# Performance work log

Measured on AMD Instinct MI355X. Metric: run time of the kernel, lower is better.

The kernel has to match this reference:

```python
import jax, jax.numpy as jnp
import numpy as np

B, Q, K, C, H = 4, 1024, 1024, 1024, 16
L = C            # latent_dim (== in_dim per module construction)
CH = L // H      # head_dim = 64


def _ln(x, w, b):
    m = jnp.mean(x, -1, keepdims=True)
    v = jnp.mean((x - m) ** 2, -1, keepdims=True)
    return (x - m) * jax.lax.rsqrt(v + 1e-5) * w + b


def setup_inputs() -> dict:
    key = jax.random.key(0)
    ks = jax.random.split(key, 16)
    s = 0.02
    return {
        "queries": jax.random.normal(ks[0], (B, Q, C), jnp.float32),
        "contexts": jax.random.normal(ks[1], (B, K, C), jnp.float32),
        "queries_hidden": jax.random.normal(ks[2], (B, Q, L), jnp.float32),
        "sa_norm_w": jnp.ones((C,), jnp.float32),
        "sa_norm_b": jnp.zeros((C,), jnp.float32),
        "sa_qkv_w": jax.random.normal(ks[3], (C, 2 * L + C), jnp.float32) * s,
        "sa_out_w": jax.random.normal(ks[4], (C, C), jnp.float32) * s,
        "sa_out_b": jnp.zeros((C,), jnp.float32),
        "ca_norm_w": jnp.ones((C,), jnp.float32),
        "ca_norm_b": jnp.zeros((C,), jnp.float32),
        "gru_w_ih": jax.random.normal(ks[5], (3 * L, C), jnp.float32) * s,
        "gru_w_hh": jax.random.normal(ks[6], (3 * L, L), jnp.float32) * s,
        "gru_b_ih": jnp.zeros((3 * L,), jnp.float32),
        "gru_b_hh": jnp.zeros((3 * L,), jnp.float32),
        "ca_k_w": jax.random.normal(ks[7], (C, L), jnp.float32) * s,
        "ca_v_w": jax.random.normal(ks[8], (C, C), jnp.float32) * s,
        "ca_out_w": jax.random.normal(ks[9], (C, C), jnp.float32) * s,
        "ca_out_b": jnp.zeros((C,), jnp.float32),
        "ln1_w": jnp.ones((C,), jnp.float32),
        "ln1_b": jnp.zeros((C,), jnp.float32),
        "lin1_w": jax.random.normal(ks[10], (C, 2 * C), jnp.float32) * s,
        "ln2_w": jnp.ones((2 * C,), jnp.float32),
        "ln2_b": jnp.zeros((2 * C,), jnp.float32),
        "lin2_w": jax.random.normal(ks[11], (2 * C, C), jnp.float32) * s,
    }


def reference(queries, contexts, queries_hidden,
              sa_norm_w, sa_norm_b, sa_qkv_w, sa_out_w, sa_out_b,
              ca_norm_w, ca_norm_b, gru_w_ih, gru_w_hh, gru_b_ih, gru_b_hh,
              ca_k_w, ca_v_w, ca_out_w, ca_out_b,
              ln1_w, ln1_b, lin1_w, ln2_w, ln2_b, lin2_w):
    scale = 1.0 / jnp.sqrt(jnp.asarray(C, queries.dtype))

    # ---- SelfAttention (pre-norm, residual) ----
    xn = _ln(queries, sa_norm_w, sa_norm_b)
    qkv = (xn @ sa_qkv_w).reshape(B, Q, H, -1)          # [B,Q,H, 2*CH + C/H]
    q, k, v = jnp.split(qkv, [CH, 2 * CH], axis=-1)
    e = jnp.einsum('nqhc,nkhc->nhqk', q, k) * scale
    a = jax.nn.softmax(e, axis=-1)
    o = jnp.einsum('nhqk,nkhc->nqhc', a, v).reshape(B, Q, C)
    x = o @ sa_out_w + sa_out_b + queries

    # ---- AttentionDynamicQuery (GRU-updated queries, cross-attn) ----
    x_pre = x
    xn = _ln(x, ca_norm_w, ca_norm_b)
    xf = xn.reshape(B * Q, C)
    hf = queries_hidden.reshape(B * Q, L)
    gi = xf @ gru_w_ih.T + gru_b_ih                     # [BQ, 3L]
    gh = hf @ gru_w_hh.T + gru_b_hh
    gir, giz, gin = jnp.split(gi, 3, axis=-1)
    ghr, ghz, ghn = jnp.split(gh, 3, axis=-1)
    r = jax.nn.sigmoid(gir + ghr)
    z = jax.nn.sigmoid(giz + ghz)
    n = jnp.tanh(gin + r * ghn)
    h = (1.0 - z) * n + z * hf                          # PyTorch GRUCell update
    qh = h.reshape(B, Q, H, CH)                         # new queries_hidden

    kk = (contexts @ ca_k_w).reshape(B, K, H, CH)
    vv = (contexts @ ca_v_w).reshape(B, K, H, C // H)
    energy = jnp.einsum('nqhc,nkhc->nhqk', qh, kk)      # returned UNscaled
    att = jax.nn.softmax(energy * scale, axis=-1)
    o = jnp.einsum('nhqk,nkhc->nqhc', att, vv).reshape(B, Q, C)
    x = o @ ca_out_w + ca_out_b + x_pre

    # ---- MLP: LN -> SiLU -> Linear -> LN -> SiLU -> Linear, residual ----
    m = jax.nn.silu(_ln(x, ln1_w, ln1_b)) @ lin1_w
    m = jax.nn.silu(_ln(m, ln2_w, ln2_b)) @ lin2_w
    out = x + m                                         # dropout(p=0) = identity
    return (out, energy, qh)
```

## Files before the change

kernel.cpp:

```cpp
#include <hip/hip_runtime.h>
#include <hip/hip_bf16.h>
#include <math.h>

static constexpr float SCALE = 0.03125f;

typedef __attribute__((ext_vector_type(4))) float f32x4;
typedef __attribute__((ext_vector_type(8))) __bf16 bf16x8;
typedef __attribute__((ext_vector_type(4))) __bf16 bf16x4;

__device__ __forceinline__ void g2l16(const void* g, void* l) {
  __builtin_amdgcn_global_load_lds(
      (const __attribute__((address_space(1))) unsigned int*)g,
      (__attribute__((address_space(3))) unsigned int*)l,
      16, 0, 0);
}

__device__ __forceinline__ void wtrans_tile(
    const float* __restrict__ src, __bf16* __restrict__ dst,
    int Kd, int N, int tid, float (*tile)[65]) {
  int t = threadIdx.x;
  int ntx = N >> 6;
  int n0 = (tid % ntx) * 64, k0 = (tid / ntx) * 64;
  #pragma unroll
  for (int i = 0; i < 16; ++i) {
    int idx = i * 256 + t; int r = idx >> 6, c = idx & 63;
    tile[r][c] = src[(size_t)(k0 + r) * N + n0 + c];
  }
  __syncthreads();
  #pragma unroll
  for (int i = 0; i < 16; ++i) {
    int idx = i * 256 + t; int r = idx >> 6, c = idx & 63;
    dst[(size_t)(n0 + r) * Kd + k0 + c] = (__bf16)tile[c][r];
  }
}

__global__ __launch_bounds__(256) void prep_crit(
    const float* __restrict__ sa_qkv_w,
    const float* __restrict__ queries, const float* __restrict__ sa_norm_w,
    const float* __restrict__ sa_norm_b,
    __bf16* __restrict__ qkvT, __bf16* __restrict__ xnB) {
  int bid = blockIdx.x;
  int t = threadIdx.x;
  if (bid < 768) {
    __shared__ float tile[64][65];
    wtrans_tile(sa_qkv_w, qkvT, 1024, 3072, bid, tile);
    return;
  }
  int row = bid - 768;
  int c = t * 4;
  float4 v = *(const float4*)(queries + (size_t)row * 1024 + c);
  float s = v.x + v.y + v.z + v.w;
  float s2 = v.x*v.x + v.y*v.y + v.z*v.z + v.w*v.w;
  #pragma unroll
  for (int off = 32; off > 0; off >>= 1) {
    s += __shfl_xor(s, off);
    s2 += __shfl_xor(s2, off);
  }
  __shared__ float red[4], red2[4];
  int wv = t >> 6;
  if ((t & 63) == 0) { red[wv] = s; red2[wv] = s2; }
  __syncthreads();
  float S  = red[0] + red[1] + red[2] + red[3];
  float S2 = red2[0] + red2[1] + red2[2] + red2[3];
  float mean = S / 1024.f;
  float var = S2 / 1024.f - mean * mean;
  float rs = rsqrtf(var + 1e-5f);
  float vv[4] = {v.x, v.y, v.z, v.w};
  bf16x4 o;
  #pragma unroll
  for (int j = 0; j < 4; ++j)
    o[j] = (__bf16)((vv[j] - mean) * rs * sa_norm_w[c+j] + sa_norm_b[c+j]);
  *(bf16x4*)(xnB + (size_t)row * 1024 + c) = o;
}

template <int NV>
__global__ __launch_bounds__(256) void ln_bf16(
    const float* __restrict__ xf, const __bf16* __restrict__ xb,
    const float* __restrict__ w, const float* __restrict__ b,
    __bf16* __restrict__ out, int silu) {
  const int D = NV * 1024;
  int row = blockIdx.x, t = threadIdx.x;
  float vals[NV * 4];
  float s = 0.f, s2 = 0.f;
  #pragma unroll
  for (int i = 0; i < NV; ++i) {
    int c = (i * 256 + t) * 4;
    float4 v;
    if (xf) {
      v = *(const float4*)(xf + (size_t)row * D + c);
    } else {
      bf16x4 vb = *(const bf16x4*)(xb + (size_t)row * D + c);
      v = make_float4((float)vb[0], (float)vb[1], (float)vb[2], (float)vb[3]);
    }
    vals[i*4+0] = v.x; vals[i*4+1] = v.y; vals[i*4+2] = v.z; vals[i*4+3] = v.w;
    s += v.x + v.y + v.z + v.w;
    s2 += v.x*v.x + v.y*v.y + v.z*v.z + v.w*v.w;
  }
  #pragma unroll
  for (int off = 32; off > 0; off >>= 1) {
    s += __shfl_xor(s, off);
    s2 += __shfl_xor(s2, off);
  }
  __shared__ float red[4], red2[4];
  int wv = t >> 6;
  if ((t & 63) == 0) { red[wv] = s; red2[wv] = s2; }
  __syncthreads();
  float S  = red[0] + red[1] + red[2] + red[3];
  float S2 = red2[0] + red2[1] + red2[2] + red2[3];
  float mean = S / D;
  float var = S2 / D - mean * mean;
  float rs = rsqrtf(var + 1e-5f);
  #pragma unroll
  for (int i = 0; i < NV; ++i) {
    int c = (i * 256 + t) * 4;
    bf16x4 o;
    #pragma unroll
    for (int j = 0; j < 4; ++j) {
      float v = (vals[i*4+j] - mean) * rs * w[c+j] + b[c+j];
      if (silu) v = v / (1.f + __expf(-v));
      o[j] = (__bf16)v;
    }
    *(bf16x4*)(out + (size_t)row * D + c) = o;
  }
}

__device__ __forceinline__ void gemm_body(
    __bf16* __restrict__ sm,
    const __bf16* __restrict__ A, long long lda,
    const __bf16* __restrict__ B, long long ldb,
    float* __restrict__ outF, __bf16* __restrict__ outB, long long ldc,
    const float* __restrict__ bias, const float* __restrict__ res,
    int K, int bm, int bn, __bf16* __restrict__ VTout, int vmode) {
  __bf16* Asm0 = sm;
  __bf16* Bsm0 = sm + 8192;
  __bf16* Asm1 = sm + 16384;
  __bf16* Bsm1 = sm + 24576;
  int t = threadIdx.x;
  int lane = t & 63, w = t >> 6;
  int l15 = lane & 15, kg = lane >> 4;
  int wm = (w >> 1) * 64, wn = (w & 1) * 64;

  f32x4 acc[4][4];
  #pragma unroll
  for (int i = 0; i < 4; ++i)
    #pragma unroll
    for (int j = 0; j < 4; ++j) acc[i][j] = (f32x4)(0.0f);

  const __bf16* ga[4]; const __bf16* gb[4];
  int lo[4];
  #pragma unroll
  for (int i = 0; i < 4; ++i) {
    int slot = i * 256 + t;
    int row = slot >> 3, s = slot & 7;
    int sx = s ^ (row & 7);
    ga[i] = A + (size_t)(bm + row) * lda + (sx << 3);
    gb[i] = B + (size_t)(bn + row) * ldb + (sx << 3);
    lo[i] = (i * 256 + w * 64) << 3;
  }

  auto STAGE = [&](__bf16* As, __bf16* Bs, int k0) {
    #pragma unroll
    for (int i = 0; i < 4; ++i) g2l16(ga[i] + k0, As + lo[i]);
    #pragma unroll
    for (int i = 0; i < 4; ++i) g2l16(gb[i] + k0, Bs + lo[i]);
  };
  auto COMPUTE = [&](const __bf16* As, const __bf16* Bs) {
    #pragma unroll
    for (int kk = 0; kk < 2; ++kk) {
      bf16x8 af[4], bfr[4];
      #pragma unroll
      for (int mi = 0; mi < 4; ++mi) {
        int row = wm + mi * 16 + l15;
        int ks = kk * 4 + kg;
        af[mi] = *(const bf16x8*)(As + row * 64 + ((ks ^ (row & 7)) << 3));
      }
      #pragma unroll
      for (int ni = 0; ni < 4; ++ni) {
        int row = wn + ni * 16 + l15;
        int ks = kk * 4 + kg;
        bfr[ni] = *(const bf16x8*)(Bs + row * 64 + ((ks ^ (row & 7)) << 3));
      }
      #pragma unroll
      for (int mi = 0; mi < 4; ++mi)
        #pragma unroll
        for (int ni = 0; ni < 4; ++ni)
          acc[mi][ni] = __builtin_amdgcn_mfma_f32_16x16x32_bf16(
              af[mi], bfr[ni], acc[mi][ni], 0, 0, 0);
    }
  };
  #define GEMM_SYNC() do { \
    asm volatile("s_waitcnt vmcnt(0)" ::: "memory"); \
    __builtin_amdgcn_s_barrier(); \
    __builtin_amdgcn_sched_barrier(0); \
  } while (0)

  STAGE(Asm0, Bsm0, 0);
  GEMM_SYNC();
  int nk = K >> 6;
  for (int kt = 0; kt + 2 < nk; kt += 2) {
    STAGE(Asm1, Bsm1, (kt + 1) << 6);
    COMPUTE(Asm0, Bsm0);
    GEMM_SYNC();
    STAGE(Asm0, Bsm0, (kt + 2) << 6);
    COMPUTE(Asm1, Bsm1);
    GEMM_SYNC();
  }
  STAGE(Asm1, Bsm1, (nk - 1) << 6);
  COMPUTE(Asm0, Bsm0);
  GEMM_SYNC();
  COMPUTE(Asm1, Bsm1);
  #undef GEMM_SYNC

  int cw = bn + wn;
  int isV = 0;
  if (vmode == 1)      isV = (cw % 192) == 128;
  else if (vmode == 2) isV = cw >= 1024;

  if (isV) {
    int h = (vmode == 1) ? (cw / 192) : ((cw - 1024) >> 6);
    int rowb = bm + wm;
    int b = rowb >> 10, k0 = rowb & 1023;
    __bf16* scr = (w < 2 ? Asm0 : Bsm0) + (w & 1) * 4096;
    #pragma unroll
    for (int mi = 0; mi < 4; ++mi) {
      #pragma unroll
      for (int ni = 0; ni < 4; ++ni) {
        int d = ni * 16 + l15;
        int sw = (d & 7) << 3;
        #pragma unroll
        for (int r = 0; r < 4; ++r) {
          int kl = mi * 16 + kg * 4 + r;
          scr[d * 64 + (kl ^ sw)] = (__bf16)acc[mi][ni][r];
        }
      }
    }
    #pragma unroll
    for (int i = 0; i < 8; ++i) {
      int idx = i * 64 + lane;
      int d = idx >> 3, kc = (idx & 7) * 8;
      bf16x8 v = *(const bf16x8*)&scr[d * 64 + (kc ^ ((d & 7) << 3))];
      *(bf16x8*)(VTout + ((size_t)((b * 16 + h) * 64 + d) << 10) + k0 + kc) = v;
    }
    return;
  }

  #pragma unroll
  for (int mi = 0; mi < 4; ++mi) {
    #pragma unroll
    for (int ni = 0; ni < 4; ++ni) {
      int rbase = bm + wm + mi * 16 + kg * 4;
      int c = bn + wn + ni * 16 + l15;
      #pragma unroll
      for (int r = 0; r < 4; ++r) {
        float val = acc[mi][ni][r];
        if (bias) val += bias[c];
        size_t off = (size_t)(rbase + r) * ldc + c;
        if (res) val += res[off];
        if (outF) outF[off] = val;
        if (outB) outB[off] = (__bf16)val;
      }
    }
  }
}

__global__ __launch_bounds__(256) void gemm_bf16(
    const __bf16* __restrict__ A, long long lda,
    const __bf16* __restrict__ B, long long ldb,
    float* __restrict__ outF, __bf16* __restrict__ outB, long long ldc,
    const float* __restrict__ bias, const float* __restrict__ res, int K,
    __bf16* __restrict__ VTout, int vmode) {
  __shared__ __bf16 sm[32768];
  int nwg = gridDim.x * gridDim.y;
  int orig = blockIdx.y * gridDim.x + blockIdx.x;
  int swz = (orig & 7) * (nwg >> 3) + (orig >> 3);
  gemm_body(sm, A, lda, B, ldb, outF, outB, ldc, bias, res, K,
            (swz / gridDim.x) * 128, (swz % gridDim.x) * 128, VTout, vmode);
}

__global__ __launch_bounds__(256) void gemm_dual(
    const __bf16* __restrict__ A0, long long lda0, const __bf16* __restrict__ B0, long long ldb0,
    float* __restrict__ oF0, __bf16* __restrict__ oB0, long long ldc0,
    const float* __restrict__ bias0, const float* __restrict__ res0, int K0, int gx0, int nb0,
    const __bf16* __restrict__ A1, long long lda1, const __bf16* __restrict__ B1, long long ldb1,
    float* __restrict__ oF1, __bf16* __restrict__ oB1, long long ldc1,
    const float* __restrict__ bias1, const float* __restrict__ res1, int K1, int gx1,
    __bf16* __restrict__ VT1, int vm1) {
  __shared__ __bf16 sm[32768];
  int bid = blockIdx.x;
  if (bid < nb0) {
    int swz = (bid & 7) * (nb0 >> 3) + (bid >> 3);
    gemm_body(sm, A0, lda0, B0, ldb0, oF0, oB0, ldc0, bias0, res0, K0,
              (swz / gx0) * 128, (swz % gx0) * 128, nullptr, 0);
  } else {
    int b = bid - nb0;
    int nb1 = gridDim.x - nb0;
    int swz = (b & 7) * (nb1 >> 3) + (b >> 3);
    gemm_body(sm, A1, lda1, B1, ldb1, oF1, oB1, ldc1, bias1, res1, K1,
              (swz / gx1) * 128, (swz % gx1) * 128, VT1, vm1);
  }
}

__global__ __launch_bounds__(256) void gemm_prep(
    const __bf16* __restrict__ Aq, const __bf16* __restrict__ Bq,
    __bf16* __restrict__ Cq, __bf16* __restrict__ VTq,
    const float* __restrict__ ca_k_w, const float* __restrict__ ca_v_w,
    const float* __restrict__ sa_out_w, const float* __restrict__ ca_out_w,
    const float* __restrict__ lin1_w, const float* __restrict__ lin2_w,
    const float* __restrict__ gru_w_ih, const float* __restrict__ gru_w_hh,
    const float* __restrict__ qhid, const float* __restrict__ contexts,
    __bf16* __restrict__ kT, __bf16* __restrict__ vT, __bf16* __restrict__ saoT,
    __bf16* __restrict__ caoT, __bf16* __restrict__ lin1T, __bf16* __restrict__ lin2T,
    __bf16* __restrict__ ihB, __bf16* __restrict__ hhB,
    __bf16* __restrict__ qhB, __bf16* __restrict__ ctxB) {
  __shared__ __bf16 sm[32768];
  int bid = blockIdx.x;
  int t = threadIdx.x;
  if (bid < 768) {
    int swz = (bid & 7) * 96 + (bid >> 3);
    gemm_body(sm, Aq, 1024, Bq, 1024, nullptr, Cq, 3072, nullptr, nullptr, 1024,
              (swz / 24) * 128, (swz % 24) * 128, VTq, 1);
    return;
  }
  if (bid >= 2816) {
    const float* csrc; __bf16* cdst; int cbase;
    if (bid < 4352)      { csrc = gru_w_ih; cdst = ihB;  cbase = 2816; }
    else if (bid < 5888) { csrc = gru_w_hh; cdst = hhB;  cbase = 4352; }
    else if (bid < 7936) { csrc = qhid;     cdst = qhB;  cbase = 5888; }
    else                 { csrc = contexts; cdst = ctxB; cbase = 7936; }
    size_t idx = ((size_t)(bid - cbase) * 256 + t) * 8;
    float4 a = *(const float4*)(csrc + idx);
    float4 b = *(const float4*)(csrc + idx + 4);
    bf16x8 o = {(__bf16)a.x,(__bf16)a.y,(__bf16)a.z,(__bf16)a.w,
                (__bf16)b.x,(__bf16)b.y,(__bf16)b.z,(__bf16)b.w};
    *(bf16x8*)(cdst + idx) = o;
    return;
  }
  const float* src; __bf16* dst; int Kd, N, base;
  if (bid < 1024)      { src = ca_k_w;   dst = kT;    Kd = 1024; N = 1024; base = 768; }
  else if (bid < 1280) { src = ca_v_w;   dst = vT;    Kd = 1024; N = 1024; base = 1024; }
  else if (bid < 1536) { src = sa_out_w; dst = saoT;  Kd = 1024; N = 1024; base = 1280; }
  else if (bid < 1792) { src = ca_out_w; dst = caoT;  Kd = 1024; N = 1024; base = 1536; }
  else if (bid < 2304) { src = lin1_w;   dst = lin1T; Kd = 1024; N = 2048; base = 1792; }
  else                 { src = lin2_w;   dst = lin2T; Kd = 2048; N = 1024; base = 2304; }
  wtrans_tile(src, dst, Kd, N, bid - base, (float(*)[65])sm);
}

__global__ __launch_bounds__(256) void gru_kernel(
    const __bf16* __restrict__ gi, const __bf16* __restrict__ gh,
    const float* __restrict__ hf, float* __restrict__ qh, __bf16* __restrict__ qhb) {
  size_t e0 = ((size_t)blockIdx.x * 256 + threadIdx.x) * 8;
  int row = (int)(e0 >> 10), col = (int)(e0 & 1023);
  size_t base = (size_t)row * 3072 + col;
  bf16x8 vir = *(const bf16x8*)(gi + base);
  bf16x8 viz = *(const bf16x8*)(gi + base + 1024);
  bf16x8 vin = *(const bf16x8*)(gi + base + 2048);
  bf16x8 vhr = *(const bf16x8*)(gh + base);
  bf16x8 vhz = *(const bf16x8*)(gh + base + 1024);
  bf16x8 vhn = *(const bf16x8*)(gh + base + 2048);
  float4 h0 = *(const float4*)(hf + e0);
  float4 h1 = *(const float4*)(hf + e0 + 4);
  float hv[8] = {h0.x, h0.y, h0.z, h0.w, h1.x, h1.y, h1.z, h1.w};
  float q[8];
  #pragma unroll
  for (int j = 0; j < 8; ++j) {
    float r = 1.f / (1.f + __expf(-((float)vir[j] + (float)vhr[j])));
    float z = 1.f / (1.f + __expf(-((float)viz[j] + (float)vhz[j])));
    float n = tanhf((float)vin[j] + r * (float)vhn[j]);
    q[j] = (1.f - z) * n + z * hv[j];
  }
  *(float4*)(qh + e0)     = make_float4(q[0], q[1], q[2], q[3]);
  *(float4*)(qh + e0 + 4) = make_float4(q[4], q[5], q[6], q[7]);
  bf16x8 qb;
  #pragma unroll
  for (int j = 0; j < 8; ++j) qb[j] = (__bf16)q[j];
  *(bf16x8*)(qhb + e0) = qb;
}

template <int E>
__global__ __launch_bounds__(256) void flash_attn(
    const __bf16* __restrict__ Qb, long long q_sb, long long q_sh, int q_sm,
    const __bf16* __restrict__ Kb, long long k_sb, long long k_sh, int k_sm,
    const __bf16* __restrict__ VT, __bf16* __restrict__ Ob,
    float* __restrict__ energyOut, float scale) {
  __shared__ __bf16 Ksm[3][4096];
  __shared__ __bf16 Vsm[3][4096];
  __shared__ __bf16 Psm[128 * 64];
  __shared__ float corr_l[128];
  __shared__ float l_l[128];
  int g = blockIdx.y, b = g >> 4, h = g & 15;
  int qt = blockIdx.x * 128;
  const __bf16* Qg = Qb + (size_t)b * q_sb + (size_t)h * q_sh;
  const __bf16* Kg = Kb + (size_t)b * k_sb + (size_t)h * k_sh;
  const __bf16* Vg = VT + (size_t)g * 65536;
  int t = threadIdx.x, lane = t & 63, w = t >> 6;
  int l15 = lane & 15, kg = lane >> 4;
  int wq = w * 32;

  bf16x8 qf[2][2];
  #pragma unroll
  for (int nq = 0; nq < 2; ++nq)
    #pragma unroll
    for (int kk = 0; kk < 2; ++kk)
      qf[nq][kk] = *(const bf16x8*)(
          Qg + (size_t)(qt + wq + nq * 16 + l15) * q_sm + kk * 32 + kg * 8);

  f32x4 acc_o[2][4];
  #pragma unroll
  for (int i = 0; i < 2; ++i)
    #pragma unroll
    for (int j = 0; j < 4; ++j) acc_o[i][j] = (f32x4)(0.0f);
  float m_run[2] = {-1e30f, -1e30f};
  float l_run[2] = {0.f, 0.f};

  const __bf16* gK[2]; const __bf16* gV[2];
  int lo[2];
  #pragma unroll
  for (int i = 0; i < 2; ++i) {
    int slot = i * 256 + t;
    int row = slot >> 3, s = slot & 7, sx = s ^ (row & 7);
    gK[i] = Kg + (size_t)row * k_sm + (sx << 3);
    gV[i] = Vg + (size_t)row * 1024 + (sx << 3);
    lo[i] = (i * 256 + w * 64) << 3;
  }

  #pragma unroll
  for (int i = 0; i < 2; ++i) g2l16(gK[i], &Ksm[0][lo[i]]);
  #pragma unroll
  for (int i = 0; i < 2; ++i) g2l16(gV[i], &Vsm[0][lo[i]]);
  #pragma unroll
  for (int i = 0; i < 2; ++i) g2l16(gK[i] + (size_t)64 * k_sm, &Ksm[1][lo[i]]);
  #pragma unroll
  for (int i = 0; i < 2; ++i) g2l16(gV[i] + 64, &Vsm[1][lo[i]]);

  int rb = 0;
  for (int kvt = 0; kvt < 16; ++kvt) {
    if (E) {
      if (kvt == 0)       asm volatile("s_waitcnt vmcnt(4)" ::: "memory");
      else if (kvt == 1)  asm volatile("s_waitcnt vmcnt(12)" ::: "memory");
      else if (kvt == 15) asm volatile("s_waitcnt vmcnt(16)" ::: "memory");
      else                asm volatile("s_waitcnt vmcnt(20)" ::: "memory");
    } else {
      if (kvt == 15)      asm volatile("s_waitcnt vmcnt(0)" ::: "memory");
      else                asm volatile("s_waitcnt vmcnt(4)" ::: "memory");
    }
    __builtin_amdgcn_s_barrier();
    __builtin_amdgcn_sched_barrier(0);

    if (kvt < 14) {
      int sbuf = rb >= 1 ? rb - 1 : rb + 2;
      size_t ko = (size_t)(kvt + 2) << 6;
      #pragma unroll
      for (int i = 0; i < 2; ++i) g2l16(gK[i] + ko * k_sm, &Ksm[sbuf][lo[i]]);
      #pragma unroll
      for (int i = 0; i < 2; ++i) g2l16(gV[i] + ko, &Vsm[sbuf][lo[i]]);
    }
    const __bf16* Ks = Ksm[rb];
    const __bf16* Vs = Vsm[rb];

    f32x4 accs[4][2];
    #pragma unroll
    for (int i = 0; i < 4; ++i)
      #pragma unroll
      for (int j = 0; j < 2; ++j) accs[i][j] = (f32x4)(0.0f);
    __builtin_amdgcn_s_setprio(1);
    #pragma unroll
    for (int tt = 0; tt < 4; ++tt) {
      bf16x8 kf[2];
      #pragma unroll
      for (int kk = 0; kk < 2; ++kk) {
        int row = tt * 16 + l15;
        int ks = kk * 4 + kg;
        kf[kk] = *(const bf16x8*)(Ks + row * 64 + ((ks ^ (row & 7)) << 3));
      }
      #pragma unroll
      for (int nq = 0; nq < 2; ++nq)
        #pragma unroll
        for (int kk = 0; kk < 2; ++kk)
          accs[tt][nq] = __builtin_amdgcn_mfma_f32_16x16x32_bf16(
              kf[kk], qf[nq][kk], accs[tt][nq], 0, 0, 0);
    }
    __builtin_amdgcn_s_setprio(0);

    if (E) {
      int kv0 = kvt << 6;
      float* eg = energyOut + ((size_t)g << 20);
      #pragma unroll
      for (int nq = 0; nq < 2; ++nq) {
        int q = qt + wq + nq * 16 + l15;
        #pragma unroll
        for (int tt = 0; tt < 4; ++tt)
          __builtin_nontemporal_store(
              accs[tt][nq], (f32x4*)(eg + (size_t)q * 1024 + kv0 + tt * 16 + kg * 4));
      }
    }

    #pragma unroll
    for (int nq = 0; nq < 2; ++nq) {
      float tmax = -1e30f;
      #pragma unroll
      for (int tt = 0; tt < 4; ++tt)
        #pragma unroll
        for (int r = 0; r < 4; ++r) tmax = fmaxf(tmax, accs[tt][nq][r]);
      tmax *= scale;
      tmax = fmaxf(tmax, __shfl_xor(tmax, 16));
      tmax = fmaxf(tmax, __shfl_xor(tmax, 32));
      float m_new = fmaxf(m_run[nq], tmax);
      float corr = __expf(m_run[nq] - m_new);
      m_run[nq] = m_new;
      int q = wq + nq * 16 + l15;
      float psum = 0.f;
      #pragma unroll
      for (int tt = 0; tt < 4; ++tt) {
        bf16x4 p4;
        #pragma unroll
        for (int r = 0; r < 4; ++r) {
          float p = __expf(accs[tt][nq][r] * scale - m_new);
          psum += p;
          p4[r] = (__bf16)p;
        }
        int kvs = (tt * 16 + kg * 4) ^ ((q & 7) << 3);
        *(bf16x4*)(Psm + q * 64 + kvs) = p4;
      }
      psum += __shfl_xor(psum, 16);
      psum += __shfl_xor(psum, 32);
      l_run[nq] = l_run[nq] * corr + psum;
      if (kg == 0) corr_l[q] = corr;
    }

    #pragma unroll
    for (int mq = 0; mq < 2; ++mq) {
      f32x4 c4 = *(const f32x4*)&corr_l[wq + mq * 16 + kg * 4];
      #pragma unroll
      for (int nd = 0; nd < 4; ++nd)
        #pragma unroll
        for (int r = 0; r < 4; ++r) acc_o[mq][nd][r] *= c4[r];
    }
    __builtin_amdgcn_s_setprio(1);
    #pragma unroll
    for (int kk = 0; kk < 2; ++kk) {
      bf16x8 pf[2], vf[4];
      #pragma unroll
      for (int mq = 0; mq < 2; ++mq) {
        int row = wq + mq * 16 + l15;
        int kvs = (kk * 32 + kg * 8) ^ ((row & 7) << 3);
        pf[mq] = *(const bf16x8*)(Psm + row * 64 + kvs);
      }
      #pragma unroll
      for (int nd = 0; nd < 4; ++nd) {
        int vrow = nd * 16 + l15;
        vf[nd] = *(const bf16x8*)(Vs + vrow * 64 + (((kk * 4 + kg) ^ (vrow & 7)) << 3));
      }
      #pragma unroll
      for (int mq = 0; mq < 2; ++mq)
        #pragma unroll
        for (int nd = 0; nd < 4; ++nd)
          acc_o[mq][nd] = __builtin_amdgcn_mfma_f32_16x16x32_bf16(
              pf[mq], vf[nd], acc_o[mq][nd], 0, 0, 0);
    }
    __builtin_amdgcn_s_setprio(0);
    rb = rb == 2 ? 0 : rb + 1;
  }

  #pragma unroll
  for (int nq = 0; nq < 2; ++nq)
    if (kg == 0) l_l[wq + nq * 16 + l15] = l_run[nq];
  __syncthreads();

  #pragma unroll
  for (int mq = 0; mq < 2; ++mq) {
    f32x4 lv = *(const f32x4*)&l_l[wq + mq * 16 + kg * 4];
    #pragma unroll
    for (int nd = 0; nd < 4; ++nd) {
      int col = h * 64 + nd * 16 + l15;
      #pragma unroll
      for (int r = 0; r < 4; ++r) {
        int qrow = qt + wq + mq * 16 + kg * 4 + r;
        Ob[(size_t)(b * 1024 + qrow) * 1024 + col] = (__bf16)(acc_o[mq][nd][r] / lv[r]);
      }
    }
  }
}

extern "C" void kernel_launch(void* const* d_in, const int* in_sizes, int n_in,
                              void* d_out, int out_size, void* d_ws, size_t ws_size,
                              hipStream_t stream) {
  (void)in_sizes; (void)n_in; (void)out_size; (void)ws_size;
  const float* queries   = (const float*)d_in[0];
  const float* contexts  = (const float*)d_in[1];
  const float* qhid      = (const float*)d_in[2];
  const float* sa_norm_w = (const float*)d_in[3];
  const float* sa_norm_b = (const float*)d_in[4];
  const float* sa_qkv_w  = (const float*)d_in[5];
  const float* sa_out_w  = (const float*)d_in[6];
  const float* sa_out_b  = (const float*)d_in[7];
  const float* ca_norm_w = (const float*)d_in[8];
  const float* ca_norm_b = (const float*)d_in[9];
  const float* gru_w_ih  = (const float*)d_in[10];
  const float* gru_w_hh  = (const float*)d_in[11];
  const float* gru_b_ih  = (const float*)d_in[12];
  const float* gru_b_hh  = (const float*)d_in[13];
  const float* ca_k_w    = (const float*)d_in[14];
  const float* ca_v_w    = (const float*)d_in[15];
  const float* ca_out_w  = (const float*)d_in[16];
  const float* ca_out_b  = (const float*)d_in[17];
  const float* ln1_w     = (const float*)d_in[18];
  const float* ln1_b     = (const float*)d_in[19];
  const float* lin1_w    = (const float*)d_in[20];
  const float* ln2_w     = (const float*)d_in[21];
  const float* ln2_b     = (const float*)d_in[22];
  const float* lin2_w    = (const float*)d_in[23];

  float* out0   = (float*)d_out;
  float* energy = out0 + (size_t)4194304;
  float* qh_out = out0 + (size_t)71303168;

  const size_t MM = 1u << 20;
  float* ws = (float*)d_ws;
  float*  X     = ws;
  float*  X2    = ws + 4 * MM;
  __bf16* M1B    = (__bf16*)(ws + 9 * MM);
  __bf16* XN_b   = (__bf16*)(ws + 17 * MM);
  __bf16* QHID_b = (__bf16*)(ws + 19 * MM);
  __bf16* CTX_b  = (__bf16*)(ws + 21 * MM);
  __bf16* O_b    = (__bf16*)(ws + 23 * MM);
  __bf16* VT_b   = (__bf16*)(ws + 25 * MM);
  __bf16* QKV_b  = (__bf16*)(ws + 27 * MM);
  __bf16* KV_b   = (__bf16*)(ws + 27 * MM);
  __bf16* LN2_b  = (__bf16*)(ws);
  __bf16* qkvT   = (__bf16*)(ws + 33 * MM);
  __bf16* ihB    = (__bf16*)(ws + 34 * MM + MM / 2);
  __bf16* hhB    = (__bf16*)(ws + 36 * MM);
  __bf16* kT     = (__bf16*)(ws + 37 * MM + MM / 2);
  __bf16* vT     = (__bf16*)(ws + 38 * MM);
  __bf16* saoT   = (__bf16*)(ws + 38 * MM + MM / 2);
  __bf16* caoT   = (__bf16*)(ws + 39 * MM);
  __bf16* lin1T  = (__bf16*)(ws + 39 * MM + MM / 2);
  __bf16* lin2T  = (__bf16*)(ws + 40 * MM + MM / 2);
  __bf16* GI_b = (__bf16*)energy;
  __bf16* GH_b = (__bf16*)(energy + 6 * MM);

  const long long QKV_SB = 1024LL * 3072;
  const long long KV_SB  = 1024LL * 2048;

  prep_crit<<<4864, 256, 0, stream>>>(
      sa_qkv_w, queries, sa_norm_w, sa_norm_b, qkvT, XN_b);

  gemm_prep<<<9984, 256, 0, stream>>>(
      XN_b, qkvT, QKV_b, VT_b,
      ca_k_w, ca_v_w, sa_out_w, ca_out_w, lin1_w, lin2_w,
      gru_w_ih, gru_w_hh, qhid, contexts,
      kT, vT, saoT, caoT, lin1T, lin2T, ihB, hhB, QHID_b, CTX_b);
  flash_attn<0><<<dim3(8, 64), 256, 0, stream>>>(
      QKV_b, QKV_SB, 192, 3072, QKV_b + 64, QKV_SB, 192, 3072,
      VT_b, O_b, nullptr, SCALE);
  gemm_dual<<<1024, 256, 0, stream>>>(
      O_b, 1024, saoT, 1024, X, nullptr, 1024, sa_out_b, queries, 1024, 8, 256,
      QHID_b, 1024, hhB, 1024, nullptr, GH_b, 3072, gru_b_hh, nullptr, 1024, 24,
      nullptr, 0);

  ln_bf16<1><<<4096, 256, 0, stream>>>(X, nullptr, ca_norm_w, ca_norm_b, XN_b, 0);
  gemm_dual<<<1280, 256, 0, stream>>>(
      XN_b, 1024, ihB, 1024, nullptr, GI_b, 3072, gru_b_ih, nullptr, 1024, 24, 768,
      CTX_b, 1024, kT, 1024, nullptr, KV_b, 2048, nullptr, nullptr, 1024, 16,
      VT_b, 2);
  gru_kernel<<<2048, 256, 0, stream>>>(GI_b, GH_b, qhid, qh_out, QHID_b );

  flash_attn<1><<<dim3(8, 64), 256, 0, stream>>>(
      QHID_b, 1024LL * 1024, 64, 1024, KV_b, KV_SB, 64, 2048,
      VT_b, O_b, energy, SCALE);
  gemm_bf16<<<dim3(8, 32), 256, 0, stream>>>(
      O_b, 1024, caoT, 1024, X2, nullptr, 1024, ca_out_b, X, 1024, nullptr, 0);

  ln_bf16<1><<<4096, 256, 0, stream>>>(X2, nullptr, ln1_w, ln1_b, XN_b, 1);
  gemm_bf16<<<dim3(16, 32), 256, 0, stream>>>(
      XN_b, 1024, lin1T, 1024, nullptr, M1B, 2048, nullptr, nullptr, 1024, nullptr, 0);
  ln_bf16<2><<<4096, 256, 0, stream>>>(nullptr, M1B, ln2_w, ln2_b, LN2_b, 1);
  gemm_bf16<<<dim3(8, 32), 256, 0, stream>>>(
      LN2_b, 2048, lin2T, 2048, out0, nullptr, 1024, nullptr, X2, 2048, nullptr, 0);
}
```

Measured before the change: 591.0 us.

## Move energy output out of cross-attention into a fused lin2 GEMM launch

The cross-attention flash kernel no longer writes the 256MB fp32 energy tensor. Instead, a new combined kernel runs the final lin2 GEMM on 256 blocks alongside 512 extra blocks that recompute Q·K^T and stream the energy out with nontemporal stores. The aim is to take the bandwidth-heavy energy write off the attention critical path and overlap it with the compute-bound GEMM. The cost is recomputing the QK products, and GEMM blocks share the device with store-heavy blocks.

New measurement: 574.1 us (median of 2 runs). 2.8% less time.

```diff
diff --git a/kernel.cpp b/kernel.cpp
--- a/kernel.cpp
+++ b/kernel.cpp
@@ -578,6 +578,111 @@
         Ob[(size_t)(b * 1024 + qrow) * 1024 + col] = (__bf16)(acc_o[mq][nd][r] / lv[r]);
       }
     }
+  }
+}
+
+__device__ __forceinline__ void energy_body(
+    __bf16* __restrict__ Ksmb,
+    const __bf16* __restrict__ Qb, long long q_sb, long long q_sh, int q_sm,
+    const __bf16* __restrict__ Kb, long long k_sb, long long k_sh, int k_sm,
+    float* __restrict__ energyOut, int g, int qt) {
+  int b = g >> 4, h = g & 15;
+  const __bf16* Qg = Qb + (size_t)b * q_sb + (size_t)h * q_sh;
+  const __bf16* Kg = Kb + (size_t)b * k_sb + (size_t)h * k_sh;
+  int t = threadIdx.x, lane = t & 63, w = t >> 6;
+  int l15 = lane & 15, kg = lane >> 4;
+  int wq = w * 32;
+
+  bf16x8 qf[2][2];
+  #pragma unroll
+  for (int nq = 0; nq < 2; ++nq)
+    #pragma unroll
+    for (int kk = 0; kk < 2; ++kk)
+      qf[nq][kk] = *(const bf16x8*)(
+          Qg + (size_t)(qt + wq + nq * 16 + l15) * q_sm + kk * 32 + kg * 8);
+
+  const __bf16* gK[2];
+  int lo[2];
+  #pragma unroll
+  for (int i = 0; i < 2; ++i) {
+    int slot = i * 256 + t;
+    int row = slot >> 3, s = slot & 7, sx = s ^ (row & 7);
+    gK[i] = Kg + (size_t)row * k_sm + (sx << 3);
+    lo[i] = (i * 256 + w * 64) << 3;
+  }
+  #pragma unroll
+  for (int i = 0; i < 2; ++i) g2l16(gK[i], Ksmb + lo[i]);
+  #pragma unroll
+  for (int i = 0; i < 2; ++i) g2l16(gK[i] + (size_t)64 * k_sm, Ksmb + 4096 + lo[i]);
+
+  float* eg = energyOut + ((size_t)g << 20);
+  int rb = 0;
+  for (int kvt = 0; kvt < 16; ++kvt) {
+    if (kvt == 0)       asm volatile("s_waitcnt vmcnt(2)" ::: "memory");
+    else if (kvt == 1)  asm volatile("s_waitcnt vmcnt(10)" ::: "memory");
+    else if (kvt == 15) asm volatile("s_waitcnt vmcnt(16)" ::: "memory");
+    else                asm volatile("s_waitcnt vmcnt(18)" ::: "memory");
+    __builtin_amdgcn_s_barrier();
+    __builtin_amdgcn_sched_barrier(0);
+
+    if (kvt < 14) {
+      int sbuf = rb >= 1 ? rb - 1 : rb + 2;
+      size_t ko = (size_t)(kvt + 2) << 6;
+      #pragma unroll
+      for (int i = 0; i < 2; ++i) g2l16(gK[i] + ko * k_sm, Ksmb + sbuf * 4096 + lo[i]);
+    }
+    const __bf16* Ks = Ksmb + rb * 4096;
+
+    f32x4 accs[4][2];
+    #pragma unroll
+    for (int i = 0; i < 4; ++i)
+      #pragma unroll
+      for (int j = 0; j < 2; ++j) accs[i][j] = (f32x4)(0.0f);
+    #pragma unroll
+    for (int tt = 0; tt < 4; ++tt) {
+      bf16x8 kf[2];
+      #pragma unroll
+      for (int kk = 0; kk < 2; ++kk) {
+        int row = tt * 16 + l15;
+        int ks = kk * 4 + kg;
+        kf[kk] = *(const bf16x8*)(Ks + row * 64 + ((ks ^ (row & 7)) << 3));
+      }
+      #pragma unroll
+      for (int nq = 0; nq < 2; ++nq)
+        #pragma unroll
+        for (int kk = 0; kk < 2; ++kk)
+          accs[tt][nq] = __builtin_amdgcn_mfma_f32_16x16x32_bf16(
+              kf[kk], qf[nq][kk], accs[tt][nq], 0, 0, 0);
+    }
+    int kv0 = kvt << 6;
+    #pragma unroll
+    for (int nq = 0; nq < 2; ++nq) {
+      int q = qt + wq + nq * 16 + l15;
+      #pragma unroll
+      for (int tt = 0; tt < 4; ++tt)
+        __builtin_nontemporal_store(
+            accs[tt][nq], (f32x4*)(eg + (size_t)q * 1024 + kv0 + tt * 16 + kg * 4));
+    }
+    rb = rb == 2 ? 0 : rb + 1;
+  }
+}
+
+__global__ __launch_bounds__(256) void gemm_lin2_energy(
+    const __bf16* __restrict__ A, const __bf16* __restrict__ B,
+    float* __restrict__ outF, const float* __restrict__ res,
+    const __bf16* __restrict__ Qb, const __bf16* __restrict__ Kb,
+    float* __restrict__ energyOut) {
+  __shared__ __bf16 sm[32768];
+  int bid = blockIdx.x;
+  if (bid < 256) {
+    int swz = (bid & 7) * 32 + (bid >> 3);
+    gemm_body(sm, A, 2048, B, 2048, outF, nullptr, 1024, nullptr, res, 2048,
+              (swz / 8) * 128, (swz % 8) * 128, nullptr, 0);
+  } else {
+    int eb = bid - 256;
+    int g = eb & 63, qt = (eb >> 6) * 128;
+    energy_body(sm, Qb, 1024LL * 1024, 64, 1024, Kb, 1024LL * 2048, 64, 2048,
+                energyOut, g, qt);
   }
 }
 
@@ -665,9 +770,9 @@
       VT_b, 2);
   gru_kernel<<<2048, 256, 0, stream>>>(GI_b, GH_b, qhid, qh_out, QHID_b );
 
-  flash_attn<1><<<dim3(8, 64), 256, 0, stream>>>(
+  flash_attn<0><<<dim3(8, 64), 256, 0, stream>>>(
       QHID_b, 1024LL * 1024, 64, 1024, KV_b, KV_SB, 64, 2048,
-      VT_b, O_b, energy, SCALE);
+      VT_b, O_b, nullptr, SCALE);
   gemm_bf16<<<dim3(8, 32), 256, 0, stream>>>(
       O_b, 1024, caoT, 1024, X2, nullptr, 1024, ca_out_b, X, 1024, nullptr, 0);
 
@@ -675,6 +780,6 @@
   gemm_bf16<<<dim3(16, 32), 256, 0, stream>>>(
       XN_b, 1024, lin1T, 1024, nullptr, M1B, 2048, nullptr, nullptr, 1024, nullptr, 0);
   ln_bf16<2><<<4096, 256, 0, stream>>>(nullptr, M1B, ln2_w, ln2_b, LN2_b, 1);
-  gemm_bf16<<<dim3(8, 32), 256, 0, stream>>>(
-      LN2_b, 2048, lin2T, 2048, out0, nullptr, 1024, nullptr, X2, 2048, nullptr, 0);
-}
+  gemm_lin2_energy<<<768, 256, 0, stream>>>(
+      LN2_b, lin2T, out0, X2, QHID_b, KV_b, energy);
+}
```
